# Kernel tuning notes

Measured on AMD Instinct MI355X. Metric: run time of the kernel, lower is better.

The kernel has to match this reference:

```python
import jax, jax.numpy as jnp
import numpy as np

D_MODEL = 1024
NUM_HEADS = 16
D_HEAD = D_MODEL // NUM_HEADS
B, S = 2, 2048


def setup_inputs() -> dict:
    key = jax.random.key(0)
    ks = jax.random.split(key, 9)
    s = 1.0 / np.sqrt(D_MODEL)
    return {
        "query": jax.random.normal(ks[0], (B, S, D_MODEL), dtype=jnp.float32),
        "key": jax.random.normal(ks[1], (B, S, D_MODEL), dtype=jnp.float32),
        "value": jax.random.normal(ks[2], (B, S, D_MODEL), dtype=jnp.float32),
        "Wq": jax.random.normal(ks[3], (D_MODEL, D_MODEL), dtype=jnp.float32) * s,
        "bq": jnp.zeros((D_MODEL,), dtype=jnp.float32),
        "Wk": jax.random.normal(ks[4], (D_MODEL, D_MODEL), dtype=jnp.float32) * s,
        "bk": jnp.zeros((D_MODEL,), dtype=jnp.float32),
        "Wv": jax.random.normal(ks[5], (D_MODEL, D_MODEL), dtype=jnp.float32) * s,
        "bv": jnp.zeros((D_MODEL,), dtype=jnp.float32),
    }


def reference(query, key, value, Wq, bq, Wk, bk, Wv, bv):
    b, sq, d = query.shape
    sk = key.shape[1]
    h, dh = NUM_HEADS, D_HEAD
    # nn.Linear: x @ W^T + b, then split heads
    q = (query @ Wq.T + bq).reshape(b, sq, h, dh)
    k = (key @ Wk.T + bk).reshape(b, sk, h, dh)
    v = (value @ Wv.T + bv).reshape(b, sk, h, dh)
    # scaled dot-product attention: scores = QK^T / sqrt(d_head)
    scores = jnp.einsum("bqhd,bkhd->bhqk", q, k) / np.sqrt(dh).astype(np.float32)
    attn = jax.nn.softmax(scores, axis=-1)  # [b, h, sq, sk]
    ctx = jnp.einsum("bhqk,bkhd->bqhd", attn, v)
    context = ctx.reshape(b, sq, h * dh)
    # original returns attn flattened heads-major: (num_heads*batch, sq, sk)
    attn_out = jnp.transpose(attn, (1, 0, 2, 3)).reshape(h * b, sq, sk)
    return context, attn_out
```

## Files before the change

kernel.cpp:

```cpp
#include <hip/hip_runtime.h>


typedef __attribute__((ext_vector_type(8))) short bf16x8;
typedef __attribute__((ext_vector_type(4))) float f32x4;

#define MFMA16(a, b, c) __builtin_amdgcn_mfma_f32_16x16x32_bf16((a), (b), (c), 0, 0, 0)

static __device__ __forceinline__ unsigned short f2bf(float x) {
    __bf16 b = (__bf16)x;
    return __builtin_bit_cast(unsigned short, b);
}
static __device__ __forceinline__ float bf2f(unsigned short s) {
    return __builtin_bit_cast(float, ((unsigned int)s) << 16);
}

static __device__ __forceinline__ void gload16(const unsigned short* g, unsigned short* l) {
    __builtin_amdgcn_global_load_lds(
        (const __attribute__((address_space(1))) unsigned int*)g,
        (__attribute__((address_space(3))) unsigned int*)l, 16, 0, 0);
}

__global__ __launch_bounds__(256, 3) void qkv_proj(
    const float* __restrict__ query, const float* __restrict__ key_, const float* __restrict__ value,
    const float* __restrict__ Wq, const float* __restrict__ bq,
    const float* __restrict__ Wk, const float* __restrict__ bk,
    const float* __restrict__ Wv, const float* __restrict__ bv,
    unsigned short* __restrict__ qb_ws, unsigned short* __restrict__ kb_ws,
    unsigned short* __restrict__ vt_ws)
{
    __shared__ unsigned short smem1[16896];
    unsigned short* const sA = smem1;
    unsigned short* const sB = smem1 + 5120;
    unsigned short* const sT = smem1;

    const int z = blockIdx.z;
    const float* __restrict__ X    = (z == 0) ? query : (z == 1) ? key_ : value;
    const float* __restrict__ W    = (z == 0) ? Wq    : (z == 1) ? Wk   : Wv;
    const float* __restrict__ bias = (z == 0) ? bq    : (z == 1) ? bk   : bv;

    const int t = threadIdx.x;
    const int l = t & 63;
    const int w = t >> 6;
    const int lr = l & 15;
    const int lk = (l >> 4) * 8;
    const int m0 = blockIdx.y * 128;
    const int n0 = blockIdx.x * 128;
    const int wr = (w >> 1) * 64;
    const int wc = (w & 1) * 64;
    const int srow = t >> 1;
    const int sc0 = (t & 1) * 16;

    f32x4 acc[4][4];
#pragma unroll
    for (int i = 0; i < 4; i++)
#pragma unroll
        for (int j = 0; j < 4; j++) acc[i][j] = (f32x4){0.f, 0.f, 0.f, 0.f};

    float4 fa[4], fb[4];
#pragma unroll
    for (int u = 0; u < 4; u++) {
        fa[u] = *(const float4*)(&X[(size_t)(m0 + srow) * 1024 + sc0 + 4 * u]);
        fb[u] = *(const float4*)(&W[(size_t)(n0 + srow) * 1024 + sc0 + 4 * u]);
    }

    for (int kk = 0; kk < 1024; kk += 32) {
        __syncthreads();
#pragma unroll
        for (int u = 0; u < 4; u++) {
            ushort4 ah, bh;
            ah.x = f2bf(fa[u].x); ah.y = f2bf(fa[u].y);
            ah.z = f2bf(fa[u].z); ah.w = f2bf(fa[u].w);
            bh.x = f2bf(fb[u].x); bh.y = f2bf(fb[u].y);
            bh.z = f2bf(fb[u].z); bh.w = f2bf(fb[u].w);
            const int si = srow * 40 + sc0 + 4 * u;
            *(ushort4*)(&sA[si]) = ah;
            *(ushort4*)(&sB[si]) = bh;
        }
        __syncthreads();
        if (kk + 32 < 1024) {
#pragma unroll
            for (int u = 0; u < 4; u++) {
                fa[u] = *(const float4*)(&X[(size_t)(m0 + srow) * 1024 + kk + 32 + sc0 + 4 * u]);
                fb[u] = *(const float4*)(&W[(size_t)(n0 + srow) * 1024 + kk + 32 + sc0 + 4 * u]);
            }
        }
        bf16x8 Ah[4], Bh[4];
#pragma unroll
        for (int i = 0; i < 4; i++) {
            Ah[i] = *(const bf16x8*)(&sA[(wr + i * 16 + lr) * 40 + lk]);
            Bh[i] = *(const bf16x8*)(&sB[(wc + i * 16 + lr) * 40 + lk]);
        }
        __builtin_amdgcn_s_setprio(1);
#pragma unroll
        for (int i = 0; i < 4; i++)
#pragma unroll
            for (int j = 0; j < 4; j++)
                acc[i][j] = MFMA16(Ah[i], Bh[j], acc[i][j]);
        __builtin_amdgcn_s_setprio(0);
    }

    if (z == 2) {
        __syncthreads();
#pragma unroll
        for (int i = 0; i < 4; i++)
#pragma unroll
            for (int j = 0; j < 4; j++) {
                const int gcol_l = wc + j * 16 + lr;
                const float bb = bias[n0 + gcol_l];
                ushort4 pk;
                pk.x = f2bf(acc[i][j][0] + bb);
                pk.y = f2bf(acc[i][j][1] + bb);
                pk.z = f2bf(acc[i][j][2] + bb);
                pk.w = f2bf(acc[i][j][3] + bb);
                *(ushort4*)(&sT[gcol_l * 132 + wr + i * 16 + (l >> 4) * 4]) = pk;
            }
        __syncthreads();
#pragma unroll
        for (int s2 = 0; s2 < 16; s2++) {
            const int rowl = s2 * 8 + (t >> 5);
            const int coll = (t & 31) * 4;
            *(ushort4*)(&vt_ws[(size_t)(n0 + rowl) * 4096 + m0 + coll]) =
                *(const ushort4*)(&sT[rowl * 132 + coll]);
        }
    } else {
#pragma unroll
        for (int i = 0; i < 4; i++)
#pragma unroll
            for (int j = 0; j < 4; j++) {
                const int gcol = n0 + wc + j * 16 + lr;
                const float bb = bias[gcol];
                const int grow0 = m0 + wr + i * 16 + (l >> 4) * 4;
                if (z == 1) {
#pragma unroll
                    for (int r = 0; r < 4; r++)
                        kb_ws[(size_t)(grow0 + r) * 1024 + gcol] = f2bf(acc[i][j][r] + bb);
                } else {
#pragma unroll
                    for (int r = 0; r < 4; r++)
                        qb_ws[(size_t)(grow0 + r) * 1024 + gcol] =
                            f2bf((acc[i][j][r] + bb) * 0.1803368801111244f);
                }
            }
    }
}

static __device__ __forceinline__ void stageK64(
    const unsigned short* __restrict__ kb_ws, unsigned short* dst,
    int b, int h, int k0, int w, int l)
{
    const int row = w * 8 + (l >> 3);
    const int col = ((l & 7) * 8) ^ ((row & 7) << 3);
    gload16(&kb_ws[(size_t)(b * 2048 + k0 + row) * 1024 + h * 64 + col], &dst[w * 512]);
}
static __device__ __forceinline__ void stageV64(
    const unsigned short* __restrict__ vt_ws, unsigned short* dst,
    int b, int h, int k0, int w, int l)
{
    const int d = w * 8 + (l >> 3);
    const int kk = ((l & 7) * 8) ^ ((d & 7) << 3);
    gload16(&vt_ws[(size_t)(h * 64 + d) * 4096 + b * 2048 + k0 + kk], &dst[w * 512]);
}
static __device__ __forceinline__ void stageWin256(
    const unsigned short* __restrict__ kb_ws, unsigned short* dst,
    int b, int h, int k0, int w, int l)
{
#pragma unroll
    for (int u = 0; u < 4; u++) {
        const int row = w * 32 + u * 8 + (l >> 3);
        const int col = ((l & 7) * 8) ^ ((row & 7) << 3);
        gload16(&kb_ws[(size_t)(b * 2048 + k0 + row) * 1024 + h * 64 + col],
                &dst[w * 2048 + u * 512]);
    }
}

static __device__ __forceinline__ void scores64(
    const unsigned short* sK, const bf16x8 (&qf)[2],
    int lr, int lg, f32x4 (&sc)[4])
{
#pragma unroll
    for (int n = 0; n < 4; n++) sc[n] = (f32x4){0.f, 0.f, 0.f, 0.f};
    __builtin_amdgcn_s_setprio(1);
#pragma unroll
    for (int n = 0; n < 4; n++) {
        const int row = n * 16 + lr;
#pragma unroll
        for (int kc = 0; kc < 2; kc++) {
            const int idx = (row * 64 + kc * 32 + lg * 8) ^ ((row & 7) << 3);
            const bf16x8 kf = *(const bf16x8*)(&sK[idx]);
            sc[n] = MFMA16(kf, qf[kc], sc[n]);
        }
    }
    __builtin_amdgcn_s_setprio(0);
}

#define SP_STRIDE 264

static __device__ __forceinline__ void doTileQKP(
    const unsigned short* sK, const unsigned short* sV, const bf16x8 (&qf)[2],
    char* sPb, f32x4 (&pv)[4], int half, int q0, int lr, int lg)
{
    f32x4 sc[4];
    scores64(sK, qf, lr, lg, sc);

    {
        char* const prow = sPb + (q0 + lr) * SP_STRIDE + half * 128;
#pragma unroll
        for (int n = 0; n < 4; n++) {
            float4 e;
            e.x = exp2f(sc[n][0]);
            e.y = exp2f(sc[n][1]);
            e.z = exp2f(sc[n][2]);
            e.w = exp2f(sc[n][3]);
            uint2 pk;
            pk.x = (unsigned int)f2bf(e.x) | ((unsigned int)f2bf(e.y) << 16);
            pk.y = (unsigned int)f2bf(e.z) | ((unsigned int)f2bf(e.w) << 16);
            *(uint2*)(prow + n * 32 + lg * 8) = pk;
        }
    }
    __builtin_amdgcn_s_setprio(1);
#pragma unroll
    for (int kcl = 0; kcl < 2; kcl++) {
        const bf16x8 pa = *(const bf16x8*)(sPb + (q0 + lr) * SP_STRIDE + half * 128 +
                                           kcl * 64 + lg * 16);
#pragma unroll
        for (int n = 0; n < 4; n++) {
            const int vrow = n * 16 + lr;
            const bf16x8 vb = *(const bf16x8*)(
                &sV[(vrow * 64 + kcl * 32 + lg * 8) ^ ((vrow & 7) << 3)]);
            pv[n] = MFMA16(pa, vb, pv[n]);
        }
    }
    __builtin_amdgcn_s_setprio(0);
}

__global__ __launch_bounds__(512, 4) void attn_fused(
    const unsigned short* __restrict__ qb_ws, const unsigned short* __restrict__ kb_ws,
    const unsigned short* __restrict__ vt_ws,
    float* __restrict__ ctx_out, float* __restrict__ attn_out)
{
    __shared__ unsigned short smem[33280];
    unsigned short* const kwin0 = smem;
    unsigned short* const kwin1 = smem + 16384;
    unsigned short* const sKA   = smem;
    unsigned short* const sKB   = smem + 4096;
    unsigned short* const sVA   = smem + 8192;
    unsigned short* const sVB   = smem + 12288;
    char* const sPb             = (char*)(smem + 16384);

    const int t = threadIdx.x;
    const int l = t & 63;
    const int w = t >> 6;
    const int lr = l & 15;
    const int lg = l >> 4;
    const int o  = (blockIdx.x & 7) * 64 + (blockIdx.x >> 3);
    const int qb = o & 15;
    const int h  = (o >> 4) & 15;
    const int b  = o >> 8;
    const int q0 = w * 16;

    bf16x8 qf[2];
    {
        const int grow = b * 2048 + qb * 128 + q0 + lr;
#pragma unroll
        for (int kc = 0; kc < 2; kc++)
            qf[kc] = *(const bf16x8*)(&qb_ws[(size_t)grow * 1024 + h * 64 + kc * 32 + lg * 8]);
    }

    float La = 0.f;

    stageWin256(kb_ws, kwin0, b, h, 0, w, l);
    __syncthreads();
    for (int kt = 0; kt < 8; kt++) {
        unsigned short* cur = (kt & 1) ? kwin1 : kwin0;
        unsigned short* nxt = (kt & 1) ? kwin0 : kwin1;
        if (kt < 7) stageWin256(kb_ws, nxt, b, h, (kt + 1) * 256, w, l);
#pragma unroll
        for (int sub = 0; sub < 4; sub++) {
            f32x4 sc[4];
            scores64(&cur[sub * 4096], qf, lr, lg, sc);
#pragma unroll
            for (int n = 0; n < 4; n++)
                La += (exp2f(sc[n][0]) + exp2f(sc[n][1])) +
                      (exp2f(sc[n][2]) + exp2f(sc[n][3]));
        }
        __syncthreads();
    }

    float invL;
    {
        float v = La;
        v += __shfl_xor(v, 16);
        v += __shfl_xor(v, 32);
        invL = 1.0f / v;
    }
    float il4[4];
#pragma unroll
    for (int i = 0; i < 4; i++) il4[i] = __shfl(invL, lg * 4 + i);
    float ilA[8];
#pragma unroll
    for (int i = 0; i < 8; i++) ilA[i] = __shfl(invL, 2 * i + (l >> 5));

    f32x4 pv[4];
#pragma unroll
    for (int n = 0; n < 4; n++) pv[n] = (f32x4){0.f, 0.f, 0.f, 0.f};

    const size_t abase = (size_t)(h * 2 + b) * 2048 + qb * 128;

    stageK64(kb_ws, sKA, b, h, 0, w, l);
    stageV64(vt_ws, sVA, b, h, 0, w, l);
    __syncthreads();
    for (int i = 0; i < 16; i++) {
        const int t0 = i * 2;
        stageK64(kb_ws, sKB, b, h, (t0 + 1) * 64, w, l);
        stageV64(vt_ws, sVB, b, h, (t0 + 1) * 64, w, l);
        doTileQKP(sKA, sVA, qf, sPb, pv, 0, q0, lr, lg);
        __syncthreads();
        if (i < 15) {
            stageK64(kb_ws, sKA, b, h, (t0 + 2) * 64, w, l);
            stageV64(vt_ws, sVA, b, h, (t0 + 2) * 64, w, l);
        }
        doTileQKP(sKB, sVB, qf, sPb, pv, 1, q0, lr, lg);
        {
            const int g0 = i * 128;
            const int rsel = l >> 5;
            const int lc = l & 31;
#pragma unroll
            for (int s = 0; s < 8; s++) {
                const int rq = q0 + 2 * s + rsel;
                ushort4 pk = *(const ushort4*)(sPb + rq * SP_STRIDE + lc * 8);
                const float il = ilA[s];
                f32x4 oo;
                oo[0] = bf2f(pk.x) * il;
                oo[1] = bf2f(pk.y) * il;
                oo[2] = bf2f(pk.z) * il;
                oo[3] = bf2f(pk.w) * il;
                __builtin_nontemporal_store(oo,
                    (f32x4*)(&attn_out[(abase + rq) * 2048 + g0 + lc * 4]));
            }
        }
        __syncthreads();
    }

#pragma unroll
    for (int r = 0; r < 4; r++) {
        const int qloc = q0 + lg * 4 + r;
        const int sq = qb * 128 + qloc;
        const float il = il4[r];
#pragma unroll
        for (int n = 0; n < 4; n++)
            __builtin_nontemporal_store(pv[n][r] * il,
                &ctx_out[((size_t)(b * 2048 + sq)) * 1024 + h * 64 + n * 16 + lr]);
    }
}

extern "C" void kernel_launch(void* const* d_in, const int* in_sizes, int n_in,
                              void* d_out, int out_size, void* d_ws, size_t ws_size,
                              hipStream_t stream)
{
    const float* query = (const float*)d_in[0];
    const float* key_  = (const float*)d_in[1];
    const float* value = (const float*)d_in[2];
    const float* Wq = (const float*)d_in[3];
    const float* bq = (const float*)d_in[4];
    const float* Wk = (const float*)d_in[5];
    const float* bk = (const float*)d_in[6];
    const float* Wv = (const float*)d_in[7];
    const float* bv = (const float*)d_in[8];

    unsigned short* qb_ws = (unsigned short*)d_ws;
    unsigned short* kb_ws = qb_ws + (size_t)4096 * 1024;
    unsigned short* vt_ws = kb_ws + (size_t)4096 * 1024;

    float* ctx_out  = (float*)d_out;
    float* attn_out = ctx_out + (size_t)2 * 2048 * 1024;

    dim3 g1(8, 32, 3);
    qkv_proj<<<g1, 256, 0, stream>>>(query, key_, value, Wq, bq, Wk, bk, Wv, bv,
                                     qb_ws, kb_ws, vt_ws);
    attn_fused<<<512, 512, 0, stream>>>(qb_ws, kb_ws, vt_ws, ctx_out, attn_out);
}
```

Measured before the change: 213.1 us.

## Load V fragments directly from global into registers instead of LDS staging

The second attention pass no longer stages V tiles into shared memory. Each wave now loads its V^T fragments straight from global memory into registers. The loop is restructured to handle one 64-key tile per iteration with a single barrier, in place of the previous two-tile unrolled loop with two barriers. This cuts LDS traffic and the number of barriers. In exchange, every wave issues redundant, less coalesced global reads of the V panel, and register pressure rises.

```diff
diff --git a/kernel.cpp b/kernel.cpp
--- a/kernel.cpp
+++ b/kernel.cpp
@@ -152,14 +152,6 @@
     const int col = ((l & 7) * 8) ^ ((row & 7) << 3);
     gload16(&kb_ws[(size_t)(b * 2048 + k0 + row) * 1024 + h * 64 + col], &dst[w * 512]);
 }
-static __device__ __forceinline__ void stageV64(
-    const unsigned short* __restrict__ vt_ws, unsigned short* dst,
-    int b, int h, int k0, int w, int l)
-{
-    const int d = w * 8 + (l >> 3);
-    const int kk = ((l & 7) * 8) ^ ((d & 7) << 3);
-    gload16(&vt_ws[(size_t)(h * 64 + d) * 4096 + b * 2048 + k0 + kk], &dst[w * 512]);
-}
 static __device__ __forceinline__ void stageWin256(
     const unsigned short* __restrict__ kb_ws, unsigned short* dst,
     int b, int h, int k0, int w, int l)
@@ -173,6 +165,18 @@
     }
 }
 
+static __device__ __forceinline__ void loadVB(
+    bf16x8 (&vb)[4][2], const unsigned short* __restrict__ vpan,
+    int k0, int lr, int lg)
+{
+#pragma unroll
+    for (int n = 0; n < 4; n++)
+#pragma unroll
+        for (int kc = 0; kc < 2; kc++)
+            vb[n][kc] = *(const bf16x8*)(
+                &vpan[(size_t)(n * 16 + lr) * 4096 + k0 + kc * 32 + lg * 8]);
+}
+
 static __device__ __forceinline__ void scores64(
     const unsigned short* sK, const bf16x8 (&qf)[2],
     int lr, int lg, f32x4 (&sc)[4])
@@ -194,44 +198,6 @@
 }
 
 #define SP_STRIDE 264
-
-static __device__ __forceinline__ void doTileQKP(
-    const unsigned short* sK, const unsigned short* sV, const bf16x8 (&qf)[2],
-    char* sPb, f32x4 (&pv)[4], int half, int q0, int lr, int lg)
-{
-    f32x4 sc[4];
-    scores64(sK, qf, lr, lg, sc);
-
-    {
-        char* const prow = sPb + (q0 + lr) * SP_STRIDE + half * 128;
-#pragma unroll
-        for (int n = 0; n < 4; n++) {
-            float4 e;
-            e.x = exp2f(sc[n][0]);
-            e.y = exp2f(sc[n][1]);
-            e.z = exp2f(sc[n][2]);
-            e.w = exp2f(sc[n][3]);
-            uint2 pk;
-            pk.x = (unsigned int)f2bf(e.x) | ((unsigned int)f2bf(e.y) << 16);
-            pk.y = (unsigned int)f2bf(e.z) | ((unsigned int)f2bf(e.w) << 16);
-            *(uint2*)(prow + n * 32 + lg * 8) = pk;
-        }
-    }
-    __builtin_amdgcn_s_setprio(1);
-#pragma unroll
-    for (int kcl = 0; kcl < 2; kcl++) {
-        const bf16x8 pa = *(const bf16x8*)(sPb + (q0 + lr) * SP_STRIDE + half * 128 +
-                                           kcl * 64 + lg * 16);
-#pragma unroll
-        for (int n = 0; n < 4; n++) {
-            const int vrow = n * 16 + lr;
-            const bf16x8 vb = *(const bf16x8*)(
-                &sV[(vrow * 64 + kcl * 32 + lg * 8) ^ ((vrow & 7) << 3)]);
-            pv[n] = MFMA16(pa, vb, pv[n]);
-        }
-    }
-    __builtin_amdgcn_s_setprio(0);
-}
 
 __global__ __launch_bounds__(512, 4) void attn_fused(
     const unsigned short* __restrict__ qb_ws, const unsigned short* __restrict__ kb_ws,
@@ -243,8 +209,6 @@
     unsigned short* const kwin1 = smem + 16384;
     unsigned short* const sKA   = smem;
     unsigned short* const sKB   = smem + 4096;
-    unsigned short* const sVA   = smem + 8192;
-    unsigned short* const sVB   = smem + 12288;
     char* const sPb             = (char*)(smem + 16384);
 
     const int t = threadIdx.x;
@@ -258,6 +222,8 @@
     const int b  = o >> 8;
     const int q0 = w * 16;
 
+    const unsigned short* __restrict__ vpan = vt_ws + (size_t)(h * 64) * 4096 + b * 2048;
+
     bf16x8 qf[2];
     {
         const int grow = b * 2048 + qb * 128 + q0 + lr;
@@ -307,21 +273,36 @@
     const size_t abase = (size_t)(h * 2 + b) * 2048 + qb * 128;
 
     stageK64(kb_ws, sKA, b, h, 0, w, l);
-    stageV64(vt_ws, sVA, b, h, 0, w, l);
     __syncthreads();
-    for (int i = 0; i < 16; i++) {
-        const int t0 = i * 2;
-        stageK64(kb_ws, sKB, b, h, (t0 + 1) * 64, w, l);
-        stageV64(vt_ws, sVB, b, h, (t0 + 1) * 64, w, l);
-        doTileQKP(sKA, sVA, qf, sPb, pv, 0, q0, lr, lg);
-        __syncthreads();
-        if (i < 15) {
-            stageK64(kb_ws, sKA, b, h, (t0 + 2) * 64, w, l);
-            stageV64(vt_ws, sVA, b, h, (t0 + 2) * 64, w, l);
-        }
-        doTileQKP(sKB, sVB, qf, sPb, pv, 1, q0, lr, lg);
+    for (int t2 = 0; t2 < 32; t2++) {
+        const int cur = t2 & 1;
+        unsigned short* const sKc = cur ? sKB : sKA;
+        unsigned short* const sKn = cur ? sKA : sKB;
+        if (t2 < 31) stageK64(kb_ws, sKn, b, h, (t2 + 1) * 64, w, l);
+
+        bf16x8 vb[4][2];
+        loadVB(vb, vpan, t2 * 64, lr, lg);
+
+        f32x4 sc[4];
+        scores64(sKc, qf, lr, lg, sc);
+
         {
-            const int g0 = i * 128;
+            char* const prow = sPb + (q0 + lr) * SP_STRIDE + cur * 128;
+#pragma unroll
+            for (int n = 0; n < 4; n++) {
+                float4 e;
+                e.x = exp2f(sc[n][0]);
+                e.y = exp2f(sc[n][1]);
+                e.z = exp2f(sc[n][2]);
+                e.w = exp2f(sc[n][3]);
+                uint2 pk;
+                pk.x = (unsigned int)f2bf(e.x) | ((unsigned int)f2bf(e.y) << 16);
+                pk.y = (unsigned int)f2bf(e.z) | ((unsigned int)f2bf(e.w) << 16);
+                *(uint2*)(prow + n * 32 + lg * 8) = pk;
+            }
+        }
+        if (cur) {
+            const int g0 = (t2 >> 1) * 128;
             const int rsel = l >> 5;
             const int lc = l & 31;
 #pragma unroll
@@ -338,6 +319,16 @@
                     (f32x4*)(&attn_out[(abase + rq) * 2048 + g0 + lc * 4]));
             }
         }
+        __builtin_amdgcn_s_setprio(1);
+#pragma unroll
+        for (int kcl = 0; kcl < 2; kcl++) {
+            const bf16x8 pa = *(const bf16x8*)(sPb + (q0 + lr) * SP_STRIDE + cur * 128 +
+                                               kcl * 64 + lg * 16);
+#pragma unroll
+            for (int n = 0; n < 4; n++)
+                pv[n] = MFMA16(pa, vb[n][kcl], pv[n]);
+        }
+        __builtin_amdgcn_s_setprio(0);
         __syncthreads();
     }
 
```

New measurement: 304.3 us. +42.8%, slower.
